# Kernel optimization log

Measured on AMD Instinct MI355X. Metric: run time of the kernel, lower is better.

The kernel has to match this reference:

```python
import math
import jax, jax.numpy as jnp
import numpy as np

B, T, C, H = 4, 2048, 1024, 16
HD = C // H  # 64


def setup_inputs() -> dict:
    key = jax.random.key(0)
    k1, k2, k3 = jax.random.split(key, 3)
    x = jax.random.normal(k1, (B, T, C), dtype=jnp.float32)
    w_attn = jax.random.normal(k2, (3 * C, C), dtype=jnp.float32) * 0.02
    w_proj = jax.random.normal(k3, (C, C), dtype=jnp.float32) * 0.02
    return {"x": x, "w_attn": w_attn, "w_proj": w_proj}


def _rms_norm(x):
    # F.rms_norm with no weight; eps defaults to dtype eps
    eps = jnp.finfo(x.dtype).eps
    return x * jax.lax.rsqrt(jnp.mean(x * x, axis=-1, keepdims=True) + eps)


def _rotary_cos_sin(seq_len, dim):
    inv_freq = 1.0 / (10000.0 ** (jnp.arange(0, dim, 2, dtype=jnp.float32) / dim))
    t = jnp.arange(seq_len, dtype=jnp.float32)
    freqs = jnp.outer(t, inv_freq)  # (T, dim//2)
    # original caches cos/sin in bfloat16
    return jnp.cos(freqs).astype(jnp.bfloat16), jnp.sin(freqs).astype(jnp.bfloat16)


def _apply_rotary(x, cos, sin):
    # x: (B, T, H, hd); cos/sin: (T, hd//2), broadcast over batch and heads
    half = x.shape[-1] // 2
    x1, x2 = x[..., :half], x[..., half:]
    c = cos[None, :, None, :].astype(x.dtype)
    s = sin[None, :, None, :].astype(x.dtype)
    y1 = x1 * c + x2 * s
    y2 = -x1 * s + x2 * c
    return jnp.concatenate([y1, y2], axis=-1)


def _forward(x, w_attn, w_proj):
    Bx, Tx, Cx = x.shape
    qkv = x @ w_attn.T  # (B, T, 3C)
    q, k, v = jnp.split(qkv, 3, axis=-1)
    q = q.reshape(Bx, Tx, H, HD)
    k = k.reshape(Bx, Tx, H, HD)
    v = v.reshape(Bx, Tx, H, HD)
    # qk RMSNorm then RoPE (nanogpt-style)
    q = _rms_norm(q)
    k = _rms_norm(k)
    cos, sin = _rotary_cos_sin(Tx, HD)
    q = _apply_rotary(q, cos, sin)
    k = _apply_rotary(k, cos, sin)
    # causal euclidean attention (custom_attention, mode='euc', dropout_p=0)
    scale = 1.0 / math.sqrt(HD)
    scores = jnp.einsum('bqhd,bkhd->bhqk', q, k) * scale  # (B, H, T, T)
    causal = jnp.tril(jnp.ones((Tx, Tx), dtype=bool))
    scores = jnp.where(causal[None, None, :, :], scores, -jnp.inf)
    attn = jax.nn.softmax(scores, axis=-1)
    y = jnp.einsum('bhqk,bkhd->bqhd', attn, v).reshape(Bx, Tx, Cx)
    return y @ w_proj.T


def reference(x, w_attn, w_proj):
    return _forward(x, w_attn, w_proj)
```

## Files before the change

### kernel.cpp

```cpp
#include <hip/hip_runtime.h>

typedef unsigned short u16;
typedef unsigned int u32;
typedef __attribute__((ext_vector_type(4))) int v4i;
typedef __attribute__((ext_vector_type(4))) float f32x4;
typedef __attribute__((ext_vector_type(16))) float f32x16;
typedef __attribute__((ext_vector_type(4))) u16 v4u;
typedef __attribute__((ext_vector_type(2))) u32 u32x2;
typedef __attribute__((ext_vector_type(8))) __bf16 bf16x8;

#define B_ 4
#define T_ 2048
#define C_ 1024
#define H_ 16
#define HD_ 64
#define C3_ 3072

__device__ __forceinline__ u16 f2b(float f) {
    unsigned u = __builtin_bit_cast(unsigned, f);
    u += 0x7FFFu + ((u >> 16) & 1u);
    return (u16)(u >> 16);
}
__device__ __forceinline__ float b2f(u16 h) {
    unsigned u = ((unsigned)h) << 16;
    return __builtin_bit_cast(float, u);
}
__device__ __forceinline__ u32 pk2(float lo, float hi) {
    __bf16 a = (__bf16)lo, b = (__bf16)hi;
    return (u32)__builtin_bit_cast(u16, a) | ((u32)__builtin_bit_cast(u16, b) << 16);
}
__device__ __forceinline__ void glds16(const u16* g, u16* l) {
    __builtin_amdgcn_global_load_lds((const __attribute__((address_space(1))) void*)g,
                                     (__attribute__((address_space(3))) void*)l, 16, 0, 0);
}
__device__ __forceinline__ float row16_sum(float v) {
    float x = v, t;
    t = __builtin_bit_cast(float, __builtin_amdgcn_update_dpp(0, __builtin_bit_cast(int, x), 0xB1, 0xF, 0xF, true));
    x += t;
    t = __builtin_bit_cast(float, __builtin_amdgcn_update_dpp(0, __builtin_bit_cast(int, x), 0x4E, 0xF, 0xF, true));
    x += t;
    t = __builtin_bit_cast(float, __builtin_amdgcn_update_dpp(0, __builtin_bit_cast(int, x), 0x141, 0xF, 0xF, true));
    x += t;
    t = __builtin_bit_cast(float, __builtin_amdgcn_update_dpp(0, __builtin_bit_cast(int, x), 0x140, 0xF, 0xF, true));
    x += t;
    return x;
}

__device__ __forceinline__ void cast4(const float* in, u16* out, int i) {
    f32x4 v = *(const f32x4*)(in + (size_t)i * 4);
    v4u o;
    o[0] = f2b(v[0]); o[1] = f2b(v[1]); o[2] = f2b(v[2]); o[3] = f2b(v[3]);
    *(v4u*)(out + (size_t)i * 4) = o;
}
__global__ __launch_bounds__(256) void prep(const float* __restrict__ x, const float* __restrict__ wa,
                                            const float* __restrict__ wp, u16* __restrict__ Xb,
                                            u16* __restrict__ Wab, u16* __restrict__ Wpb,
                                            u16* __restrict__ Rp) {
    int i = blockIdx.x * 256 + threadIdx.x;
    if (i < 2097152) { cast4(x, Xb, i); return; }
    i -= 2097152;
    if (i < 786432) { cast4(wa, Wab, i); return; }
    i -= 786432;
    if (i < 262144) { cast4(wp, Wpb, i); return; }
    i -= 262144;
    int t = i >> 5, j = i & 31;
    float invf = exp2f(-(float)j * (13.287712379549449f / 32.0f));
    float fr = (float)t * invf;
    float s, c;
    sincosf(fr, &s, &c);
    Rp[i * 2]     = f2b(c);
    Rp[i * 2 + 1] = f2b(s);
}

__device__ __forceinline__ void store_out(u16* p, float v)   { *p = f2b(v); }
__device__ __forceinline__ void store_out(float* p, float v) { *p = v; }

template <typename OutT>
__global__ __launch_bounds__(256) void gemm_bt5(const u16* __restrict__ A, const u16* __restrict__ Bm,
                                                OutT* __restrict__ Cout, int Mdim, int Ndim, int Kdim) {
    __shared__ u16 As[8192];
    __shared__ u16 Bs[8192];
    const int tid = threadIdx.x;
    const int F = blockIdx.y * gridDim.x + blockIdx.x;
    const int cpx = (gridDim.x * gridDim.y) >> 3;
    const int wg = (F & 7) * cpx + (F >> 3);
    const int row0 = (wg / gridDim.x) * 128;
    const int col0 = (wg % gridDim.x) * 128;
    const int w = tid >> 6, lane = tid & 63;
    const int wm = w >> 1, wn = w & 1;
    const int lr = lane & 15, lk = lane >> 4;

    const f32x4 zf = {0.f, 0.f, 0.f, 0.f};
    f32x4 acc[4][4];
#pragma unroll
    for (int m = 0; m < 4; m++)
#pragma unroll
        for (int n = 0; n < 4; n++) acc[m][n] = zf;

    const u16* Ab = A + (size_t)row0 * Kdim;
    const u16* Bb = Bm + (size_t)col0 * Kdim;
    const int srw = lane >> 3;
    const int gch = (lane & 7) ^ (srw & 7);
    const size_t grow[4] = {
        (size_t)(w * 32 + 0 * 8 + srw) * Kdim + gch * 8,
        (size_t)(w * 32 + 1 * 8 + srw) * Kdim + gch * 8,
        (size_t)(w * 32 + 2 * 8 + srw) * Kdim + gch * 8,
        (size_t)(w * 32 + 3 * 8 + srw) * Kdim + gch * 8 };
    const int rx = lr & 7;

    for (int k0 = 0; k0 < Kdim; k0 += 64) {
#pragma unroll
        for (int j = 0; j < 4; j++) glds16(Ab + grow[j] + k0, As + (w * 32 + j * 8) * 64);
#pragma unroll
        for (int j = 0; j < 4; j++) glds16(Bb + grow[j] + k0, Bs + (w * 32 + j * 8) * 64);
        __syncthreads();
#pragma unroll
        for (int kk = 0; kk < 2; kk++) {
            const int chx = ((kk * 4 + lk) ^ rx) * 8;
            bf16x8 af[4], bfr[4];
#pragma unroll
            for (int m = 0; m < 4; m++) af[m]  = *(const bf16x8*)&As[(wm * 64 + m * 16 + lr) * 64 + chx];
#pragma unroll
            for (int n = 0; n < 4; n++) bfr[n] = *(const bf16x8*)&Bs[(wn * 64 + n * 16 + lr) * 64 + chx];
#pragma unroll
            for (int m = 0; m < 4; m++)
#pragma unroll
                for (int n = 0; n < 4; n++)
                    acc[m][n] = __builtin_amdgcn_mfma_f32_16x16x32_bf16(af[m], bfr[n], acc[m][n], 0, 0, 0);
        }
        __syncthreads();
    }
#pragma unroll
    for (int m = 0; m < 4; m++)
#pragma unroll
        for (int n = 0; n < 4; n++) {
            const int rr = row0 + wm * 64 + m * 16 + lk * 4;
            const int cc = col0 + wn * 64 + n * 16 + lr;
#pragma unroll
            for (int j = 0; j < 4; j++)
                store_out(Cout + (size_t)(rr + j) * Ndim + cc, acc[m][n][j]);
        }
}

__global__ __launch_bounds__(256) void gemm_qkv(const u16* __restrict__ A, const u16* __restrict__ Bm,
                                                u16* __restrict__ Qn, u16* __restrict__ Kn,
                                                u16* __restrict__ Vt, const u16* __restrict__ rope) {
    const int Kdim = 1024;
    __shared__ u16 As[8192];
    __shared__ u16 Bs[8192];
    const int tid = threadIdx.x;
    const int F = blockIdx.y * gridDim.x + blockIdx.x;
    const int cpx = (gridDim.x * gridDim.y) >> 3;
    const int wg = (F & 7) * cpx + (F >> 3);
    const int row0 = (wg / gridDim.x) * 128;
    const int col0 = (wg % gridDim.x) * 128;
    const int w = tid >> 6, lane = tid & 63;
    const int wm = w >> 1, wn = w & 1;
    const int lr = lane & 15, lk = lane >> 4;

    const f32x4 zf = {0.f, 0.f, 0.f, 0.f};
    f32x4 acc[4][4];
#pragma unroll
    for (int m = 0; m < 4; m++)
#pragma unroll
        for (int n = 0; n < 4; n++) acc[m][n] = zf;

    const u16* Ab = A + (size_t)row0 * Kdim;
    const u16* Bb = Bm + (size_t)col0 * Kdim;
    const int srw = lane >> 3;
    const int gch = (lane & 7) ^ (srw & 7);
    const size_t grow[4] = {
        (size_t)(w * 32 + 0 * 8 + srw) * Kdim + gch * 8,
        (size_t)(w * 32 + 1 * 8 + srw) * Kdim + gch * 8,
        (size_t)(w * 32 + 2 * 8 + srw) * Kdim + gch * 8,
        (size_t)(w * 32 + 3 * 8 + srw) * Kdim + gch * 8 };
    const int rx = lr & 7;

    for (int k0 = 0; k0 < Kdim; k0 += 64) {
#pragma unroll
        for (int j = 0; j < 4; j++) glds16(Ab + grow[j] + k0, As + (w * 32 + j * 8) * 64);
#pragma unroll
        for (int j = 0; j < 4; j++) glds16(Bb + grow[j] + k0, Bs + (w * 32 + j * 8) * 64);
        __syncthreads();
#pragma unroll
        for (int kk = 0; kk < 2; kk++) {
            const int chx = ((kk * 4 + lk) ^ rx) * 8;
            bf16x8 af[4], bfr[4];
#pragma unroll
            for (int m = 0; m < 4; m++) af[m]  = *(const bf16x8*)&As[(wm * 64 + m * 16 + lr) * 64 + chx];
#pragma unroll
            for (int n = 0; n < 4; n++) bfr[n] = *(const bf16x8*)&Bs[(wn * 64 + n * 16 + lr) * 64 + chx];
#pragma unroll
            for (int m = 0; m < 4; m++)
#pragma unroll
                for (int n = 0; n < 4; n++)
                    acc[m][n] = __builtin_amdgcn_mfma_f32_16x16x32_bf16(af[m], bfr[n], acc[m][n], 0, 0, 0);
        }
        __syncthreads();
    }
    const u32* rp32 = (const u32*)rope;
    const int type = col0 >> 10;
    const int h = ((col0 & 1023) >> 6) + wn;
    if (type == 2) {
#pragma unroll
        for (int m = 0; m < 4; m++)
#pragma unroll
            for (int n = 0; n < 4; n++) {
                const int d = n * 16 + lr;
                const int rr0 = row0 + wm * 64 + m * 16 + lk * 4;
                const int bq = rr0 >> 11, t0 = rr0 & 2047;
                const int bh = bq * 16 + h;
                u32x2 st;
                st[0] = pk2(acc[m][n][0], acc[m][n][1]);
                st[1] = pk2(acc[m][n][2], acc[m][n][3]);
                *(u32x2*)(Vt + ((size_t)bh * HD_ + d) * T_ + t0) = st;
            }
    } else {
        u16* outb = type ? Kn : Qn;
        const float osc = type ? 1.0f : 0.18033688011112042f;
#pragma unroll
        for (int m = 0; m < 4; m++) {
            float rmsj[4];
#pragma unroll
            for (int j = 0; j < 4; j++) {
                const float ss = row16_sum(acc[m][0][j] * acc[m][0][j] + acc[m][1][j] * acc[m][1][j]
                                         + acc[m][2][j] * acc[m][2][j] + acc[m][3][j] * acc[m][3][j]);
                rmsj[j] = rsqrtf(ss * (1.f / 64.f) + 1.1920929e-7f) * osc;
            }
#pragma unroll
            for (int n = 0; n < 2; n++)
#pragma unroll
                for (int j = 0; j < 4; j++) {
                    const int d = n * 16 + lr;
                    const int rr = row0 + wm * 64 + m * 16 + lk * 4 + j;
                    const int bq = rr >> 11, t = rr & 2047;
                    const int bh = bq * 16 + h;
                    const u32 cs = rp32[t * 32 + d];
                    const float c = b2f((u16)(cs & 0xFFFFu));
                    const float s = b2f((u16)(cs >> 16));
                    const float x1 = acc[m][n][j] * rmsj[j];
                    const float x2 = acc[m][n + 2][j] * rmsj[j];
                    u16* bp = outb + ((size_t)bh * T_ + t) * HD_;
                    bp[d]      = f2b(x1 * c + x2 * s);
                    bp[d + 32] = f2b(x2 * c - x1 * s);
                }
        }
    }
}

__global__ __launch_bounds__(256, 4) void attn_fwd9(const u16* __restrict__ Qn, const u16* __restrict__ Kn,
                                                    const u16* __restrict__ Vt, u16* __restrict__ Yb) {
    __shared__ u16 Ks[2][4096];
    __shared__ u16 Vs[2][4096];
    const int tid = threadIdx.x;
    const int w = tid >> 6, lane = tid & 63, la = lane & 31, hi = lane >> 5;
    const int gid = blockIdx.x;
    const int bh = gid & 63, qb = 15 - (gid >> 6);
    const int b = bh >> 4, h = bh & 15;
    const int q0w = qb * 128 + w * 32;
    const int q = q0w + la;
    const u16* Qp = Qn + (size_t)bh * T_ * HD_;
    const u16* Kp = Kn + (size_t)bh * T_ * HD_;
    const u16* Vp = Vt + (size_t)bh * HD_ * T_;

    bf16x8 qf[4];
#pragma unroll
    for (int c = 0; c < 4; c++)
        qf[c] = *(const bf16x8*)(Qp + (size_t)q * HD_ + c * 16 + hi * 8);

    v4i oi; oi[0] = oi[1] = oi[2] = oi[3] = 0x3F803F80;
    const bf16x8 onesf = __builtin_bit_cast(bf16x8, oi);

    f32x16 O0, O1, lsum;
#pragma unroll
    for (int r = 0; r < 16; r++) { O0[r] = 0.f; O1[r] = 0.f; lsum[r] = 0.f; }
    const int lastt = q0w >> 6;
    const int ntile = 2 * qb + 2;
    const int s8 = lane >> 3;
    const int gch = (lane & 7) ^ s8;
    const int Rw = w * 16;
    const size_t kbase = (size_t)(Rw + s8) * HD_ + gch * 8;
    const size_t vbase = (size_t)(Rw + s8) * T_ + gch * 8;
    const int swl = (la & 7) << 3;

    auto STAGE = [&](int bi, int kv0) {
        glds16(Kp + kbase + (size_t)kv0 * HD_,       &Ks[bi][Rw * 64]);
        glds16(Kp + kbase + (size_t)(kv0 + 8) * HD_, &Ks[bi][Rw * 64 + 512]);
        glds16(Vp + vbase + kv0,                     &Vs[bi][Rw * 64]);
        glds16(Vp + vbase + 8 * T_ + kv0,            &Vs[bi][Rw * 64 + 512]);
    };
    auto COMPUTE = [&](int bi, int kt) {
        const int kv0 = kt * 64;
        f32x16 s0, s1;
#pragma unroll
        for (int r = 0; r < 16; r++) { s0[r] = 0.f; s1[r] = 0.f; }
#pragma unroll
        for (int c = 0; c < 4; c++) {
            const int cb = c * 16 + hi * 8;
            bf16x8 kfa = *(const bf16x8*)&Ks[bi][la * 64 + (cb ^ swl)];
            bf16x8 kfb = *(const bf16x8*)&Ks[bi][(32 + la) * 64 + (cb ^ swl)];
            s0 = __builtin_amdgcn_mfma_f32_32x32x16_bf16(kfa, qf[c], s0, 0, 0, 0);
            s1 = __builtin_amdgcn_mfma_f32_32x32x16_bf16(kfb, qf[c], s1, 0, 0, 0);
        }
        if (kt == lastt) {
#pragma unroll
            for (int r = 0; r < 16; r++) {
                const int cr = (r & 3) + 8 * (r >> 2) + 4 * hi;
                if (kv0 + cr > q)      s0[r] = -3e38f;
                if (kv0 + 32 + cr > q) s1[r] = -3e38f;
            }
        }
        float p0[16], p1[16];
#pragma unroll
        for (int r = 0; r < 16; r++) {
            p0[r] = exp2f(s0[r]);
            p1[r] = exp2f(s1[r]);
        }
#pragma unroll
        for (int g = 0; g < 2; g++) {
            u32 P2[8];
#pragma unroll
            for (int j = 0; j < 8; j++)
                P2[j] = g ? pk2(p1[2 * j], p1[2 * j + 1]) : pk2(p0[2 * j], p0[2 * j + 1]);
            auto s02 = __builtin_amdgcn_permlane32_swap((int)P2[0], (int)P2[2], false, false);
            auto s13 = __builtin_amdgcn_permlane32_swap((int)P2[1], (int)P2[3], false, false);
            auto s46 = __builtin_amdgcn_permlane32_swap((int)P2[4], (int)P2[6], false, false);
            auto s57 = __builtin_amdgcn_permlane32_swap((int)P2[5], (int)P2[7], false, false);
            v4i w0, w1;
            w0[0] = s02[0]; w0[1] = s13[0]; w0[2] = s02[1]; w0[3] = s13[1];
            w1[0] = s46[0]; w1[1] = s57[0]; w1[2] = s46[1]; w1[3] = s57[1];
            const bf16x8 pa0 = __builtin_bit_cast(bf16x8, w0);
            const bf16x8 pa1 = __builtin_bit_cast(bf16x8, w1);
            lsum = __builtin_amdgcn_mfma_f32_32x32x16_bf16(onesf, pa0, lsum, 0, 0, 0);
            lsum = __builtin_amdgcn_mfma_f32_32x32x16_bf16(onesf, pa1, lsum, 0, 0, 0);
#pragma unroll
            for (int ks = 0; ks < 2; ks++) {
                const bf16x8 pa = ks ? pa1 : pa0;
                const int cb = g * 32 + ks * 16 + hi * 8;
                bf16x8 vfa = *(const bf16x8*)&Vs[bi][la * 64 + (cb ^ swl)];
                bf16x8 vfb = *(const bf16x8*)&Vs[bi][(32 + la) * 64 + (cb ^ swl)];
                O0 = __builtin_amdgcn_mfma_f32_32x32x16_bf16(vfa, pa, O0, 0, 0, 0);
                O1 = __builtin_amdgcn_mfma_f32_32x32x16_bf16(vfb, pa, O1, 0, 0, 0);
            }
        }
    };

    STAGE(0, 0);
    for (int t = 0; t < ntile; t += 2) {
        __syncthreads();
        STAGE(1, (t + 1) * 64);
        if (t <= lastt) COMPUTE(0, t);
        __syncthreads();
        if (t + 2 < ntile) STAGE(0, (t + 2) * 64);
        if (t + 1 <= lastt) COMPUTE(1, t + 1);
    }

    const float inv = 1.f / lsum[0];
    u16* yrow = Yb + ((size_t)(b * T_) + q) * C_ + h * HD_;
#pragma unroll
    for (int r4 = 0; r4 < 4; r4++) {
        u32x2 st0, st1;
        st0[0] = pk2(O0[r4 * 4 + 0] * inv, O0[r4 * 4 + 1] * inv);
        st0[1] = pk2(O0[r4 * 4 + 2] * inv, O0[r4 * 4 + 3] * inv);
        st1[0] = pk2(O1[r4 * 4 + 0] * inv, O1[r4 * 4 + 1] * inv);
        st1[1] = pk2(O1[r4 * 4 + 2] * inv, O1[r4 * 4 + 3] * inv);
        *(u32x2*)(yrow + r4 * 8 + hi * 4)      = st0;
        *(u32x2*)(yrow + 32 + r4 * 8 + hi * 4) = st1;
    }
}

extern "C" void kernel_launch(void* const* d_in, const int* in_sizes, int n_in,
                              void* d_out, int out_size, void* d_ws, size_t ws_size,
                              hipStream_t stream) {
    const float* x      = (const float*)d_in[0];
    const float* w_attn = (const float*)d_in[1];
    const float* w_proj = (const float*)d_in[2];
    float* out = (float*)d_out;
    char* ws = (char*)d_ws;
    u16* Wpb = (u16*)(ws + 0);
    u16* Rp  = (u16*)(ws + 2097152);
    u16* Xb  = (u16*)(ws + 2359296);
    u16* Wab = (u16*)(ws + 19136512);
    u16* Qn  = (u16*)(ws + 25427968);
    u16* Kn  = (u16*)(ws + 42205184);
    u16* Vt  = (u16*)(ws + 58982400);
    u16* Yb  = (u16*)(ws + 75759616);

    prep<<<12544, 256, 0, stream>>>(x, w_attn, w_proj, Xb, Wab, Wpb, Rp);
    gemm_qkv<<<dim3(24, 64), 256, 0, stream>>>(Xb, Wab, Qn, Kn, Vt, Rp);
    attn_fwd9<<<1024, 256, 0, stream>>>(Qn, Kn, Vt, Yb);
    gemm_bt5<float><<<dim3(8, 64), 256, 0, stream>>>(Yb, Wpb, out, 8192, 1024, 1024);
}
```

Baseline: 172.2 us.

## Stage QKV epilogue through swizzled LDS for coalesced stores; grid-stride prep kernel

The QKV GEMM epilogue now writes its normalized, rotated Q/K tiles and its transposed V tile into a per-wave XOR-swizzled shared-memory buffer. It then emits 16-byte coalesced global stores in place of scattered 2-byte and 8-byte writes. This targets uncoalesced store traffic in the epilogue, at the cost of an extra barrier and an LDS round trip. The prep kernel is also changed to a grid-stride loop with 2048 blocks to cut block launch overhead.

```diff
diff --git a/kernel.cpp b/kernel.cpp
--- a/kernel.cpp
+++ b/kernel.cpp
@@ -56,20 +56,22 @@
                                             const float* __restrict__ wp, u16* __restrict__ Xb,
                                             u16* __restrict__ Wab, u16* __restrict__ Wpb,
                                             u16* __restrict__ Rp) {
-    int i = blockIdx.x * 256 + threadIdx.x;
-    if (i < 2097152) { cast4(x, Xb, i); return; }
-    i -= 2097152;
-    if (i < 786432) { cast4(wa, Wab, i); return; }
-    i -= 786432;
-    if (i < 262144) { cast4(wp, Wpb, i); return; }
-    i -= 262144;
-    int t = i >> 5, j = i & 31;
-    float invf = exp2f(-(float)j * (13.287712379549449f / 32.0f));
-    float fr = (float)t * invf;
-    float s, c;
-    sincosf(fr, &s, &c);
-    Rp[i * 2]     = f2b(c);
-    Rp[i * 2 + 1] = f2b(s);
+    for (int i0 = blockIdx.x * 256 + threadIdx.x; i0 < 3211264; i0 += 2048 * 256) {
+        int i = i0;
+        if (i < 2097152) { cast4(x, Xb, i); continue; }
+        i -= 2097152;
+        if (i < 786432) { cast4(wa, Wab, i); continue; }
+        i -= 786432;
+        if (i < 262144) { cast4(wp, Wpb, i); continue; }
+        i -= 262144;
+        int t = i >> 5, j = i & 31;
+        float invf = exp2f(-(float)j * (13.287712379549449f / 32.0f));
+        float fr = (float)t * invf;
+        float s, c;
+        sincosf(fr, &s, &c);
+        Rp[i * 2]     = f2b(c);
+        Rp[i * 2 + 1] = f2b(s);
+    }
 }
 
 __device__ __forceinline__ void store_out(u16* p, float v)   { *p = f2b(v); }
@@ -146,8 +148,9 @@
                                                 u16* __restrict__ Qn, u16* __restrict__ Kn,
                                                 u16* __restrict__ Vt, const u16* __restrict__ rope) {
     const int Kdim = 1024;
-    __shared__ u16 As[8192];
-    __shared__ u16 Bs[8192];
+    __shared__ u16 smem[16384];
+    u16* As = smem;
+    u16* Bs = smem + 8192;
     const int tid = threadIdx.x;
     const int F = blockIdx.y * gridDim.x + blockIdx.x;
     const int cpx = (gridDim.x * gridDim.y) >> 3;
@@ -198,23 +201,31 @@
         }
         __syncthreads();
     }
+    __syncthreads();
+    u16* epw = smem + w * 4096;
     const u32* rp32 = (const u32*)rope;
     const int type = col0 >> 10;
     const int h = ((col0 & 1023) >> 6) + wn;
+    const int tbase = (row0 & 2047) + wm * 64;
+    const int bh = (row0 >> 11) * 16 + h;
     if (type == 2) {
 #pragma unroll
         for (int m = 0; m < 4; m++)
 #pragma unroll
             for (int n = 0; n < 4; n++) {
                 const int d = n * 16 + lr;
-                const int rr0 = row0 + wm * 64 + m * 16 + lk * 4;
-                const int bq = rr0 >> 11, t0 = rr0 & 2047;
-                const int bh = bq * 16 + h;
-                u32x2 st;
-                st[0] = pk2(acc[m][n][0], acc[m][n][1]);
-                st[1] = pk2(acc[m][n][2], acc[m][n][3]);
-                *(u32x2*)(Vt + ((size_t)bh * HD_ + d) * T_ + t0) = st;
+#pragma unroll
+                for (int j = 0; j < 4; j++) {
+                    const int t_l = m * 16 + lk * 4 + j;
+                    epw[d * 64 + (((t_l >> 3) ^ (d & 7)) << 3) + (t_l & 7)] = f2b(acc[m][n][j]);
+                }
             }
+#pragma unroll
+        for (int c = 0; c < 8; c++) {
+            const int r = (lane >> 3) + 8 * c;
+            v4i val = *(const v4i*)&epw[r * 64 + (((lane & 7) ^ (r & 7)) << 3)];
+            *(v4i*)(Vt + ((size_t)bh * HD_ + r) * T_ + tbase + (lane & 7) * 8) = val;
+        }
     } else {
         u16* outb = type ? Kn : Qn;
         const float osc = type ? 1.0f : 0.18033688011112042f;
@@ -232,18 +243,23 @@
 #pragma unroll
                 for (int j = 0; j < 4; j++) {
                     const int d = n * 16 + lr;
-                    const int rr = row0 + wm * 64 + m * 16 + lk * 4 + j;
-                    const int bq = rr >> 11, t = rr & 2047;
-                    const int bh = bq * 16 + h;
+                    const int rowl = m * 16 + lk * 4 + j;
+                    const int t = tbase + rowl;
                     const u32 cs = rp32[t * 32 + d];
                     const float c = b2f((u16)(cs & 0xFFFFu));
                     const float s = b2f((u16)(cs >> 16));
                     const float x1 = acc[m][n][j] * rmsj[j];
                     const float x2 = acc[m][n + 2][j] * rmsj[j];
-                    u16* bp = outb + ((size_t)bh * T_ + t) * HD_;
-                    bp[d]      = f2b(x1 * c + x2 * s);
-                    bp[d + 32] = f2b(x2 * c - x1 * s);
+                    const int rxr = (rowl & 7) << 3;
+                    epw[rowl * 64 + (((d >> 3) << 3) ^ rxr) + (d & 7)]        = f2b(x1 * c + x2 * s);
+                    epw[rowl * 64 + ((((d + 32) >> 3) << 3) ^ rxr) + (d & 7)] = f2b(x2 * c - x1 * s);
                 }
+        }
+#pragma unroll
+        for (int c = 0; c < 8; c++) {
+            const int r = (lane >> 3) + 8 * c;
+            v4i val = *(const v4i*)&epw[r * 64 + (((lane & 7) ^ (r & 7)) << 3)];
+            *(v4i*)(outb + ((size_t)bh * T_ + tbase + r) * HD_ + (lane & 7) * 8) = val;
         }
     }
 }
@@ -386,7 +402,7 @@
     u16* Vt  = (u16*)(ws + 58982400);
     u16* Yb  = (u16*)(ws + 75759616);
 
-    prep<<<12544, 256, 0, stream>>>(x, w_attn, w_proj, Xb, Wab, Wpb, Rp);
+    prep<<<2048, 256, 0, stream>>>(x, w_attn, w_proj, Xb, Wab, Wpb, Rp);
     gemm_qkv<<<dim3(24, 64), 256, 0, stream>>>(Xb, Wab, Qn, Kn, Vt, Rp);
     attn_fwd9<<<1024, 256, 0, stream>>>(Qn, Kn, Vt, Yb);
     gemm_bt5<float><<<dim3(8, 64), 256, 0, stream>>>(Yb, Wpb, out, 8192, 1024, 1024);
```

After: 171.2 us. Within noise of the previous version (-0.6%).
